# Kernel optimization log

Hardware: AMD Instinct MI355X
Metric: run time of the kernel (lower is better)

## Reference

```python
import jax, jax.numpy as jnp
import numpy as np

B, S, D, UNITS = 8, 2048, 1024, 1024

def setup_inputs() -> dict:
    key = jax.random.key(0)
    k1, k2, k3, k4 = jax.random.split(key, 4)
    scale = 1.0 / np.sqrt(D)
    return {
        "inputs": jax.random.normal(k1, (B, S, D), dtype=jnp.float32),
        "Wq": jax.random.normal(k2, (D, UNITS), dtype=jnp.float32) * scale,
        "Wk": jax.random.normal(k3, (D, UNITS), dtype=jnp.float32) * scale,
        "Wv": jax.random.normal(k4, (D, UNITS), dtype=jnp.float32) * scale,
    }

def reference(inputs, Wq, Wk, Wv):
    # QKV projections (bias-free Dense): [B,S,D] @ [D,U] -> [B,S,U]
    q = jnp.einsum("bsd,du->bsu", inputs, Wq)
    k = jnp.einsum("bsd,du->bsu", inputs, Wk)
    v = jnp.einsum("bsd,du->bsu", inputs, Wv)
    # scaled dot-product scores [B,S,S]
    scores = jnp.einsum("bqu,bku->bqk", q, k) / jnp.sqrt(jnp.float32(UNITS))
    attn = jax.nn.softmax(scores, axis=-1)
    # weighted sum of values [B,S,U]
    return jnp.einsum("bqk,bku->bqu", attn, v)
```

## Files before the change

### kernel.cpp

```cpp
#include <hip/hip_runtime.h>


#define BM 128
#define BN 128
#define BK 64

typedef _Float16 half8  __attribute__((ext_vector_type(8)));
typedef _Float16 half4v __attribute__((ext_vector_type(4)));
typedef _Float16 half2v __attribute__((ext_vector_type(2)));
typedef float    floatx4 __attribute__((ext_vector_type(4)));

__device__ __forceinline__ void stage_async(const _Float16* __restrict__ src, int ld,
                                            _Float16* __restrict__ dst, int wave, int lane) {
#pragma unroll
    for (int i = 0; i < 4; ++i) {
        int chunk = i * 4 + wave;
        int L = chunk * 64 + lane;
        int row = L >> 3, c8 = L & 7;
        int cg = c8 ^ (row & 7);
        __builtin_amdgcn_global_load_lds(
            (const __attribute__((address_space(1))) unsigned int*)(src + (size_t)row * ld + cg * 8),
            (__attribute__((address_space(3))) unsigned int*)(dst + chunk * 512),
            16, 0, 0);
    }
}

__device__ __forceinline__ void mfma_accum(const _Float16* __restrict__ As,
                                           const _Float16* __restrict__ Bs,
                                           int wm, int wn, int l15, int q4,
                                           floatx4 acc[4][4]) {
#pragma unroll
    for (int kk = 0; kk < 2; ++kk) {
        half8 a[4], b[4];
#pragma unroll
        for (int i = 0; i < 4; ++i) {
            int row = wm * 64 + i * 16 + l15;
            int cg = (kk * 4 + q4) ^ (row & 7);
            a[i] = *(const half8*)(As + row * 64 + cg * 8);
        }
#pragma unroll
        for (int j = 0; j < 4; ++j) {
            int row = wn * 64 + j * 16 + l15;
            int cg = (kk * 4 + q4) ^ (row & 7);
            b[j] = *(const half8*)(Bs + row * 64 + cg * 8);
        }
#pragma unroll
        for (int i = 0; i < 4; ++i)
#pragma unroll
            for (int j = 0; j < 4; ++j)
                acc[i][j] = __builtin_amdgcn_mfma_f32_16x16x32_f16(a[i], b[j], acc[i][j], 0, 0, 0);
    }
}

__device__ __forceinline__ float sum8h(half8 a) {
    union { half8 v; half2v h2[4]; } u; u.v = a;
    half2v s0 = u.h2[0] + u.h2[1];
    half2v s1 = u.h2[2] + u.h2[3];
    half2v s  = s0 + s1;
    return (float)s[0] + (float)s[1];
}

__global__ void cast_x(const float* __restrict__ X, _Float16* __restrict__ Xh) {
    size_t i = ((size_t)blockIdx.x * 256 + threadIdx.x) * 8;
    float4 v0 = *(const float4*)(X + i);
    float4 v1 = *(const float4*)(X + i + 4);
    half8 hh;
    hh[0] = (_Float16)v0.x; hh[1] = (_Float16)v0.y; hh[2] = (_Float16)v0.z; hh[3] = (_Float16)v0.w;
    hh[4] = (_Float16)v1.x; hh[5] = (_Float16)v1.y; hh[6] = (_Float16)v1.z; hh[7] = (_Float16)v1.w;
    *(half8*)(Xh + i) = hh;
}

__global__ void prep_weights(const float* __restrict__ Wq, const float* __restrict__ Wk,
                             const float* __restrict__ Wv, _Float16* __restrict__ WbT) {
    int g = blockIdx.z;
    const float* W = (g == 0) ? Wq : (g == 1) ? Wk : Wv;
    __shared__ float tile[32][33];
    int u0 = blockIdx.x * 32, d0 = blockIdx.y * 32;
    int tx = threadIdx.x & 31, ty = threadIdx.x >> 5;
#pragma unroll
    for (int i = 0; i < 32; i += 8)
        tile[ty + i][tx] = W[(size_t)(d0 + ty + i) * 1024 + (u0 + tx)];
    __syncthreads();
#pragma unroll
    for (int i = 0; i < 32; i += 8)
        WbT[(size_t)g * 1024 * 1024 + (size_t)(u0 + ty + i) * 1024 + (d0 + tx)] =
            (_Float16)tile[tx][ty + i];
}

__global__ void qkv_gemm(const _Float16* __restrict__ Xh, const _Float16* __restrict__ WbT,
                         _Float16* __restrict__ Qh, _Float16* __restrict__ Kh,
                         _Float16* __restrict__ Vt) {
    __shared__ __align__(16) _Float16 As[BM * BK];
    __shared__ __align__(16) _Float16 Bs[BN * BK];
    int t = threadIdx.x;
    int lane = t & 63, wave = t >> 6;
    int wm = wave >> 1, wn = wave & 1;
    int l15 = lane & 15, q4 = lane >> 4;
    int m0 = blockIdx.y * BM, n0 = blockIdx.x * BN;
    floatx4 acc[4][4] = {};
    for (int kt = 0; kt < 1024; kt += BK) {
        __syncthreads();
        stage_async(Xh + (size_t)m0 * 1024 + kt, 1024, As, wave, lane);
        stage_async(WbT + (size_t)n0 * 1024 + kt, 1024, Bs, wave, lane);
        __syncthreads();
        mfma_accum(As, Bs, wm, wn, l15, q4, acc);
    }
    int which = blockIdx.x >> 3;
    int u0 = (blockIdx.x & 7) * BN;
    int b = m0 >> 11;
    int sbase = (m0 & 2047) + wm * 64;
    if (which < 2) {
        _Float16* dst = which ? Kh : Qh;
        _Float16* db = dst + (size_t)b * 2048 * 1024;
#pragma unroll
        for (int i = 0; i < 4; ++i)
#pragma unroll
            for (int j = 0; j < 4; ++j)
#pragma unroll
                for (int r = 0; r < 4; ++r) {
                    int s = sbase + i * 16 + q4 * 4 + r;
                    int u = u0 + wn * 64 + j * 16 + l15;
                    db[(size_t)s * 1024 + u] = (_Float16)acc[i][j][r];
                }
    } else {
        _Float16* vb = Vt + (size_t)b * 1024 * 2048;
#pragma unroll
        for (int i = 0; i < 4; ++i)
#pragma unroll
            for (int j = 0; j < 4; ++j) {
                int s = sbase + i * 16 + q4 * 4;
                int u = u0 + wn * 64 + j * 16 + l15;
                half4v pk;
#pragma unroll
                for (int r = 0; r < 4; ++r) pk[r] = (_Float16)acc[i][j][r];
                *(half4v*)(vb + (size_t)u * 2048 + s) = pk;
            }
    }
}

__global__ void scores_gemm(const _Float16* __restrict__ Qh, const _Float16* __restrict__ Kh,
                            _Float16* __restrict__ P) {
    __shared__ __align__(16) _Float16 As[BM * BK];
    __shared__ __align__(16) _Float16 Bs[BN * BK];
    int t = threadIdx.x;
    int lane = t & 63, wave = t >> 6;
    int wm = wave >> 1, wn = wave & 1;
    int l15 = lane & 15, q4 = lane >> 4;
    int m0 = blockIdx.y * BM, n0 = blockIdx.x * BN;
    int batch = blockIdx.z;
    const _Float16* A = Qh + (size_t)batch * 2048 * 1024;
    const _Float16* B = Kh + (size_t)batch * 2048 * 1024;
    floatx4 acc[4][4] = {};
    for (int kt = 0; kt < 1024; kt += BK) {
        __syncthreads();
        stage_async(A + (size_t)m0 * 1024 + kt, 1024, As, wave, lane);
        stage_async(B + (size_t)n0 * 1024 + kt, 1024, Bs, wave, lane);
        __syncthreads();
        mfma_accum(As, Bs, wm, wn, l15, q4, acc);
    }
    _Float16* Pb = P + (size_t)batch * 2048 * 2048;
#pragma unroll
    for (int i = 0; i < 4; ++i)
#pragma unroll
        for (int j = 0; j < 4; ++j)
#pragma unroll
            for (int r = 0; r < 4; ++r) {
                int m = m0 + wm * 64 + i * 16 + q4 * 4 + r;
                int n = n0 + wn * 64 + j * 16 + l15;
                Pb[(size_t)m * 2048 + n] = (_Float16)__expf(acc[i][j][r] * 0.03125f);
            }
}

__global__ void pv_gemm(const _Float16* __restrict__ P, const _Float16* __restrict__ Vt,
                        float* __restrict__ out) {
    __shared__ __align__(16) _Float16 As[BM * BK];
    __shared__ __align__(16) _Float16 Bs[BN * BK];
    int t = threadIdx.x;
    int lane = t & 63, wave = t >> 6;
    int wm = wave >> 1, wn = wave & 1;
    int l15 = lane & 15, q4 = lane >> 4;
    int m0 = blockIdx.y * BM, n0 = blockIdx.x * BN;
    int batch = blockIdx.z;
    const _Float16* A = P + (size_t)batch * 2048 * 2048;
    const _Float16* B = Vt + (size_t)batch * 1024 * 2048;
    floatx4 acc[4][4] = {};
    float rsum[4] = {0.f, 0.f, 0.f, 0.f};
    for (int kt = 0; kt < 2048; kt += BK) {
        __syncthreads();
        stage_async(A + (size_t)m0 * 2048 + kt, 2048, As, wave, lane);
        stage_async(B + (size_t)n0 * 2048 + kt, 2048, Bs, wave, lane);
        __syncthreads();
#pragma unroll
        for (int kk = 0; kk < 2; ++kk) {
            half8 a[4], b[4];
#pragma unroll
            for (int i = 0; i < 4; ++i) {
                int row = wm * 64 + i * 16 + l15;
                int cg = (kk * 4 + q4) ^ (row & 7);
                a[i] = *(const half8*)(As + row * 64 + cg * 8);
                rsum[i] += sum8h(a[i]);
            }
#pragma unroll
            for (int j = 0; j < 4; ++j) {
                int row = wn * 64 + j * 16 + l15;
                int cg = (kk * 4 + q4) ^ (row & 7);
                b[j] = *(const half8*)(Bs + row * 64 + cg * 8);
            }
#pragma unroll
            for (int i = 0; i < 4; ++i)
#pragma unroll
                for (int j = 0; j < 4; ++j)
                    acc[i][j] = __builtin_amdgcn_mfma_f32_16x16x32_f16(a[i], b[j], acc[i][j], 0, 0, 0);
        }
    }
    float rsumf[4];
#pragma unroll
    for (int i = 0; i < 4; ++i) {
        float v = rsum[i] + __shfl_xor(rsum[i], 16);
        rsumf[i] = v + __shfl_xor(v, 32);
    }
    float* ob = out + (size_t)batch * 2048 * 1024;
#pragma unroll
    for (int i = 0; i < 4; ++i)
#pragma unroll
        for (int r = 0; r < 4; ++r) {
            int rloc = q4 * 4 + r;
            float inv = 1.0f / __shfl(rsumf[i], rloc);
            int m = m0 + wm * 64 + i * 16 + rloc;
#pragma unroll
            for (int j = 0; j < 4; ++j) {
                int n = n0 + wn * 64 + j * 16 + l15;
                ob[(size_t)m * 1024 + n] = acc[i][j][r] * inv;
            }
        }
}

extern "C" void kernel_launch(void* const* d_in, const int* in_sizes, int n_in,
                              void* d_out, int out_size, void* d_ws, size_t ws_size,
                              hipStream_t stream) {
    const float* X  = (const float*)d_in[0];
    const float* Wq = (const float*)d_in[1];
    const float* Wk = (const float*)d_in[2];
    const float* Wv = (const float*)d_in[3];
    float* out = (float*)d_out;

    char* ws = (char*)d_ws;
    size_t off = 0;
    _Float16* Xh  = (_Float16*)(ws + off); off += (size_t)8 * 2048 * 1024 * 2;
    _Float16* WbT = (_Float16*)(ws + off); off += (size_t)3 * 1024 * 1024 * 2;
    _Float16* Qh  = (_Float16*)(ws + off); off += (size_t)8 * 2048 * 1024 * 2;
    _Float16* Kh  = (_Float16*)(ws + off); off += (size_t)8 * 2048 * 1024 * 2;
    _Float16* Vt  = (_Float16*)(ws + off); off += (size_t)8 * 1024 * 2048 * 2;
    _Float16* P   = (_Float16*)(ws + off); off += (size_t)8 * 2048 * 2048 * 2;

    cast_x      <<<dim3(8192, 1, 1), 256, 0, stream>>>(X, Xh);
    prep_weights<<<dim3(32, 32, 3), 256, 0, stream>>>(Wq, Wk, Wv, WbT);
    qkv_gemm    <<<dim3(24, 128, 1), 256, 0, stream>>>(Xh, WbT, Qh, Kh, Vt);
    scores_gemm <<<dim3(16, 16, 8),  256, 0, stream>>>(Qh, Kh, P);
    pv_gemm     <<<dim3(8, 16, 8),   256, 0, stream>>>(P, Vt, out);
}
```

Measured before the change: 394.0 us.

## Use 256x256 tiles with 8 waves and double-buffered pipelined LDS staging

Replaces the 128x128 single-buffered GEMM loop with a shared 256x256-tile, 512-thread GEMM core. It double-buffers LDS and issues global-to-LDS loads for the next two k-steps interleaved with MFMA phases, using explicit vmcnt waits, barriers and setprio. All three GEMM stages use this core, which aims to raise arithmetic intensity and hide load latency behind compute. In exchange it uses 128KB of LDS per block and more accumulator registers, launches fewer blocks (e.g. 256 for pv), and depends on carefully ordered waits for correctness.

```diff
diff --git a/kernel.cpp b/kernel.cpp
--- a/kernel.cpp
+++ b/kernel.cpp
@@ -1,54 +1,23 @@
 #include <hip/hip_runtime.h>
 
-
-#define BM 128
-#define BN 128
-#define BK 64
 
 typedef _Float16 half8  __attribute__((ext_vector_type(8)));
 typedef _Float16 half4v __attribute__((ext_vector_type(4)));
 typedef _Float16 half2v __attribute__((ext_vector_type(2)));
 typedef float    floatx4 __attribute__((ext_vector_type(4)));
 
-__device__ __forceinline__ void stage_async(const _Float16* __restrict__ src, int ld,
-                                            _Float16* __restrict__ dst, int wave, int lane) {
-#pragma unroll
-    for (int i = 0; i < 4; ++i) {
-        int chunk = i * 4 + wave;
-        int L = chunk * 64 + lane;
-        int row = L >> 3, c8 = L & 7;
+__device__ __forceinline__ void stage_ht(const _Float16* __restrict__ src, int ld,
+                                         _Float16* __restrict__ dst, int wave, int lane) {
+#pragma unroll
+    for (int i = 0; i < 2; ++i) {
+        int q = wave * 2 + i;
+        int c = q * 64 + lane;
+        int row = c >> 3, c8 = c & 7;
         int cg = c8 ^ (row & 7);
         __builtin_amdgcn_global_load_lds(
             (const __attribute__((address_space(1))) unsigned int*)(src + (size_t)row * ld + cg * 8),
-            (__attribute__((address_space(3))) unsigned int*)(dst + chunk * 512),
+            (__attribute__((address_space(3))) unsigned int*)(dst + q * 512),
             16, 0, 0);
-    }
-}
-
-__device__ __forceinline__ void mfma_accum(const _Float16* __restrict__ As,
-                                           const _Float16* __restrict__ Bs,
-                                           int wm, int wn, int l15, int q4,
-                                           floatx4 acc[4][4]) {
-#pragma unroll
-    for (int kk = 0; kk < 2; ++kk) {
-        half8 a[4], b[4];
-#pragma unroll
-        for (int i = 0; i < 4; ++i) {
-            int row = wm * 64 + i * 16 + l15;
-            int cg = (kk * 4 + q4) ^ (row & 7);
-            a[i] = *(const half8*)(As + row * 64 + cg * 8);
-        }
-#pragma unroll
-        for (int j = 0; j < 4; ++j) {
-            int row = wn * 64 + j * 16 + l15;
-            int cg = (kk * 4 + q4) ^ (row & 7);
-            b[j] = *(const half8*)(Bs + row * 64 + cg * 8);
-        }
-#pragma unroll
-        for (int i = 0; i < 4; ++i)
-#pragma unroll
-            for (int j = 0; j < 4; ++j)
-                acc[i][j] = __builtin_amdgcn_mfma_f32_16x16x32_f16(a[i], b[j], acc[i][j], 0, 0, 0);
     }
 }
 
@@ -58,6 +27,96 @@
     half2v s1 = u.h2[2] + u.h2[3];
     half2v s  = s0 + s1;
     return (float)s[0] + (float)s[1];
+}
+
+#define SA_(T, h) stage_ht(A + (size_t)((h) * 128) * lda + (size_t)(T) * 64, lda, \
+                           ShA + (((T) & 1) * 2 + (h)) * 8192, wave, lane)
+#define SB_(T, h) stage_ht(B + (size_t)((h) * 128) * ldb + (size_t)(T) * 64, ldb, \
+                           ShB + (((T) & 1) * 2 + (h)) * 8192, wave, lane)
+
+#define LOADA(aq, i0)                                                        \
+    _Pragma("unroll")                                                        \
+    for (int ii = 0; ii < 2; ++ii) {                                         \
+        int rr = ((i0) + ii) * 16 + l15;                                     \
+        _Pragma("unroll")                                                    \
+        for (int kk = 0; kk < 2; ++kk) {                                     \
+            int cg = (kk * 4 + q4) ^ (rr & 7);                               \
+            aq[ii][kk] = *(const half8*)(As + rr * 64 + cg * 8);             \
+            if (RSUM) rsum[(i0) + ii] += sum8h(aq[ii][kk]);                  \
+        }                                                                    \
+    }
+
+#define MFMAQ(aq, i0)                                                        \
+    asm volatile("s_waitcnt lgkmcnt(0)" ::: "memory");                       \
+    __builtin_amdgcn_s_setprio(1);                                           \
+    _Pragma("unroll")                                                        \
+    for (int kk = 0; kk < 2; ++kk)                                           \
+        _Pragma("unroll")                                                    \
+        for (int ii = 0; ii < 2; ++ii)                                       \
+            _Pragma("unroll")                                                \
+            for (int j = 0; j < 4; ++j)                                      \
+                acc[(i0) + ii][j] = __builtin_amdgcn_mfma_f32_16x16x32_f16(  \
+                    aq[ii][kk], b[j][kk], acc[(i0) + ii][j], 0, 0, 0);       \
+    __builtin_amdgcn_s_setprio(0);
+
+#define BARF() do { __builtin_amdgcn_s_barrier(); asm volatile("" ::: "memory"); } while (0)
+
+template<bool RSUM>
+__device__ __forceinline__ void gemm8p(const _Float16* __restrict__ A, int lda,
+                                       const _Float16* __restrict__ B, int ldb,
+                                       int K, _Float16* __restrict__ ShA,
+                                       _Float16* __restrict__ ShB,
+                                       int wave, int lane,
+                                       floatx4 (&acc)[8][4], float (&rsum)[8]) {
+    const int wm = wave >> 2, wn = wave & 3;
+    const int l15 = lane & 15, q4 = lane >> 4;
+    const int NT = K >> 6;
+
+    SB_(0, 0); SB_(0, 1); SA_(0, 1); SA_(0, 0);
+    if (NT > 1) { SB_(1, 0); SB_(1, 1); SA_(1, 1); }
+
+    for (int t = 0; t < NT; ++t) {
+        const _Float16* As = ShA + (t & 1) * 16384 + wm * 8192;
+        const _Float16* Bs = ShB + (t & 1) * 16384 + (wn >> 1) * 8192;
+        const int rb = (wn & 1) * 64;
+        half8 b[4][2];
+        half8 a0[2][2], a1[2][2], a2[2][2], a3[2][2];
+
+        if (t + 1 < NT) SA_(t + 1, 0);
+        if (t == NT - 1) asm volatile("s_waitcnt vmcnt(0)" ::: "memory");
+        else             asm volatile("s_waitcnt vmcnt(8)" ::: "memory");
+        BARF();
+#pragma unroll
+        for (int j = 0; j < 4; ++j) {
+            int rr = rb + j * 16 + l15;
+#pragma unroll
+            for (int kk = 0; kk < 2; ++kk) {
+                int cg = (kk * 4 + q4) ^ (rr & 7);
+                b[j][kk] = *(const half8*)(Bs + rr * 64 + cg * 8);
+            }
+        }
+        LOADA(a0, 0);
+        MFMAQ(a0, 0);
+        BARF();
+
+        LOADA(a1, 2);
+        if (t + 2 < NT) SB_(t + 2, 0);
+        BARF();
+        MFMAQ(a1, 2);
+        BARF();
+
+        LOADA(a2, 4);
+        LOADA(a3, 6);
+        if (t + 2 < NT) SB_(t + 2, 1);
+        BARF();
+        MFMAQ(a2, 4);
+        BARF();
+
+        if (t + 2 < NT) SA_(t + 2, 1);
+        BARF();
+        MFMAQ(a3, 6);
+        BARF();
+    }
 }
 
 __global__ void cast_x(const float* __restrict__ X, _Float16* __restrict__ Xh) {
@@ -87,33 +146,31 @@
             (_Float16)tile[tx][ty + i];
 }
 
-__global__ void qkv_gemm(const _Float16* __restrict__ Xh, const _Float16* __restrict__ WbT,
-                         _Float16* __restrict__ Qh, _Float16* __restrict__ Kh,
-                         _Float16* __restrict__ Vt) {
-    __shared__ __align__(16) _Float16 As[BM * BK];
-    __shared__ __align__(16) _Float16 Bs[BN * BK];
+__global__ __launch_bounds__(512, 2)
+void qkv_gemm(const _Float16* __restrict__ Xh, const _Float16* __restrict__ WbT,
+              _Float16* __restrict__ Qh, _Float16* __restrict__ Kh,
+              _Float16* __restrict__ Vt) {
+    __shared__ __align__(16) _Float16 ShA[32768];
+    __shared__ __align__(16) _Float16 ShB[32768];
     int t = threadIdx.x;
     int lane = t & 63, wave = t >> 6;
-    int wm = wave >> 1, wn = wave & 1;
+    int wm = wave >> 2, wn = wave & 3;
     int l15 = lane & 15, q4 = lane >> 4;
-    int m0 = blockIdx.y * BM, n0 = blockIdx.x * BN;
-    floatx4 acc[4][4] = {};
-    for (int kt = 0; kt < 1024; kt += BK) {
-        __syncthreads();
-        stage_async(Xh + (size_t)m0 * 1024 + kt, 1024, As, wave, lane);
-        stage_async(WbT + (size_t)n0 * 1024 + kt, 1024, Bs, wave, lane);
-        __syncthreads();
-        mfma_accum(As, Bs, wm, wn, l15, q4, acc);
-    }
-    int which = blockIdx.x >> 3;
-    int u0 = (blockIdx.x & 7) * BN;
-    int b = m0 >> 11;
-    int sbase = (m0 & 2047) + wm * 64;
+    int which = blockIdx.x >> 2;
+    int u0 = (blockIdx.x & 3) * 256;
+    int m0 = blockIdx.y * 256;
+    const _Float16* A = Xh + (size_t)m0 * 1024;
+    const _Float16* B = WbT + (size_t)which * 1024 * 1024 + (size_t)u0 * 1024;
+    floatx4 acc[8][4] = {};
+    float rsum[8] = {};
+    gemm8p<false>(A, 1024, B, 1024, 1024, ShA, ShB, wave, lane, acc, rsum);
+
+    int bz = m0 >> 11;
+    int sbase = (m0 & 2047) + wm * 128;
     if (which < 2) {
-        _Float16* dst = which ? Kh : Qh;
-        _Float16* db = dst + (size_t)b * 2048 * 1024;
-#pragma unroll
-        for (int i = 0; i < 4; ++i)
+        _Float16* db = (which ? Kh : Qh) + (size_t)bz * 2048 * 1024;
+#pragma unroll
+        for (int i = 0; i < 8; ++i)
 #pragma unroll
             for (int j = 0; j < 4; ++j)
 #pragma unroll
@@ -123,9 +180,9 @@
                     db[(size_t)s * 1024 + u] = (_Float16)acc[i][j][r];
                 }
     } else {
-        _Float16* vb = Vt + (size_t)b * 1024 * 2048;
-#pragma unroll
-        for (int i = 0; i < 4; ++i)
+        _Float16* vb = Vt + (size_t)bz * 1024 * 2048;
+#pragma unroll
+        for (int i = 0; i < 8; ++i)
 #pragma unroll
             for (int j = 0; j < 4; ++j) {
                 int s = sbase + i * 16 + q4 * 4;
@@ -138,95 +195,67 @@
     }
 }
 
-__global__ void scores_gemm(const _Float16* __restrict__ Qh, const _Float16* __restrict__ Kh,
-                            _Float16* __restrict__ P) {
-    __shared__ __align__(16) _Float16 As[BM * BK];
-    __shared__ __align__(16) _Float16 Bs[BN * BK];
+__global__ __launch_bounds__(512, 2)
+void scores_gemm(const _Float16* __restrict__ Qh, const _Float16* __restrict__ Kh,
+                 _Float16* __restrict__ P) {
+    __shared__ __align__(16) _Float16 ShA[32768];
+    __shared__ __align__(16) _Float16 ShB[32768];
     int t = threadIdx.x;
     int lane = t & 63, wave = t >> 6;
-    int wm = wave >> 1, wn = wave & 1;
+    int wm = wave >> 2, wn = wave & 3;
     int l15 = lane & 15, q4 = lane >> 4;
-    int m0 = blockIdx.y * BM, n0 = blockIdx.x * BN;
+    int m0 = blockIdx.y * 256, n0 = blockIdx.x * 256;
     int batch = blockIdx.z;
-    const _Float16* A = Qh + (size_t)batch * 2048 * 1024;
-    const _Float16* B = Kh + (size_t)batch * 2048 * 1024;
-    floatx4 acc[4][4] = {};
-    for (int kt = 0; kt < 1024; kt += BK) {
-        __syncthreads();
-        stage_async(A + (size_t)m0 * 1024 + kt, 1024, As, wave, lane);
-        stage_async(B + (size_t)n0 * 1024 + kt, 1024, Bs, wave, lane);
-        __syncthreads();
-        mfma_accum(As, Bs, wm, wn, l15, q4, acc);
-    }
+    const _Float16* A = Qh + (size_t)batch * 2048 * 1024 + (size_t)m0 * 1024;
+    const _Float16* B = Kh + (size_t)batch * 2048 * 1024 + (size_t)n0 * 1024;
+    floatx4 acc[8][4] = {};
+    float rsum[8] = {};
+    gemm8p<false>(A, 1024, B, 1024, 1024, ShA, ShB, wave, lane, acc, rsum);
+
     _Float16* Pb = P + (size_t)batch * 2048 * 2048;
 #pragma unroll
-    for (int i = 0; i < 4; ++i)
+    for (int i = 0; i < 8; ++i)
 #pragma unroll
         for (int j = 0; j < 4; ++j)
 #pragma unroll
             for (int r = 0; r < 4; ++r) {
-                int m = m0 + wm * 64 + i * 16 + q4 * 4 + r;
+                int m = m0 + wm * 128 + i * 16 + q4 * 4 + r;
                 int n = n0 + wn * 64 + j * 16 + l15;
                 Pb[(size_t)m * 2048 + n] = (_Float16)__expf(acc[i][j][r] * 0.03125f);
             }
 }
 
-__global__ void pv_gemm(const _Float16* __restrict__ P, const _Float16* __restrict__ Vt,
-                        float* __restrict__ out) {
-    __shared__ __align__(16) _Float16 As[BM * BK];
-    __shared__ __align__(16) _Float16 Bs[BN * BK];
+__global__ __launch_bounds__(512, 2)
+void pv_gemm(const _Float16* __restrict__ P, const _Float16* __restrict__ Vt,
+             float* __restrict__ out) {
+    __shared__ __align__(16) _Float16 ShA[32768];
+    __shared__ __align__(16) _Float16 ShB[32768];
     int t = threadIdx.x;
     int lane = t & 63, wave = t >> 6;
-    int wm = wave >> 1, wn = wave & 1;
+    int wm = wave >> 2, wn = wave & 3;
     int l15 = lane & 15, q4 = lane >> 4;
-    int m0 = blockIdx.y * BM, n0 = blockIdx.x * BN;
+    int m0 = blockIdx.y * 256, n0 = blockIdx.x * 256;
     int batch = blockIdx.z;
-    const _Float16* A = P + (size_t)batch * 2048 * 2048;
-    const _Float16* B = Vt + (size_t)batch * 1024 * 2048;
-    floatx4 acc[4][4] = {};
-    float rsum[4] = {0.f, 0.f, 0.f, 0.f};
-    for (int kt = 0; kt < 2048; kt += BK) {
-        __syncthreads();
-        stage_async(A + (size_t)m0 * 2048 + kt, 2048, As, wave, lane);
-        stage_async(B + (size_t)n0 * 2048 + kt, 2048, Bs, wave, lane);
-        __syncthreads();
-#pragma unroll
-        for (int kk = 0; kk < 2; ++kk) {
-            half8 a[4], b[4];
-#pragma unroll
-            for (int i = 0; i < 4; ++i) {
-                int row = wm * 64 + i * 16 + l15;
-                int cg = (kk * 4 + q4) ^ (row & 7);
-                a[i] = *(const half8*)(As + row * 64 + cg * 8);
-                rsum[i] += sum8h(a[i]);
-            }
-#pragma unroll
-            for (int j = 0; j < 4; ++j) {
-                int row = wn * 64 + j * 16 + l15;
-                int cg = (kk * 4 + q4) ^ (row & 7);
-                b[j] = *(const half8*)(Bs + row * 64 + cg * 8);
-            }
-#pragma unroll
-            for (int i = 0; i < 4; ++i)
-#pragma unroll
-                for (int j = 0; j < 4; ++j)
-                    acc[i][j] = __builtin_amdgcn_mfma_f32_16x16x32_f16(a[i], b[j], acc[i][j], 0, 0, 0);
-        }
-    }
-    float rsumf[4];
-#pragma unroll
-    for (int i = 0; i < 4; ++i) {
+    const _Float16* A = P + (size_t)batch * 2048 * 2048 + (size_t)m0 * 2048;
+    const _Float16* B = Vt + (size_t)batch * 1024 * 2048 + (size_t)n0 * 2048;
+    floatx4 acc[8][4] = {};
+    float rsum[8] = {};
+    gemm8p<true>(A, 2048, B, 2048, 2048, ShA, ShB, wave, lane, acc, rsum);
+
+    float rsumf[8];
+#pragma unroll
+    for (int i = 0; i < 8; ++i) {
         float v = rsum[i] + __shfl_xor(rsum[i], 16);
         rsumf[i] = v + __shfl_xor(v, 32);
     }
     float* ob = out + (size_t)batch * 2048 * 1024;
 #pragma unroll
-    for (int i = 0; i < 4; ++i)
+    for (int i = 0; i < 8; ++i)
 #pragma unroll
         for (int r = 0; r < 4; ++r) {
             int rloc = q4 * 4 + r;
             float inv = 1.0f / __shfl(rsumf[i], rloc);
-            int m = m0 + wm * 64 + i * 16 + rloc;
+            int m = m0 + wm * 128 + i * 16 + rloc;
 #pragma unroll
             for (int j = 0; j < 4; ++j) {
                 int n = n0 + wn * 64 + j * 16 + l15;
@@ -255,7 +284,7 @@
 
     cast_x      <<<dim3(8192, 1, 1), 256, 0, stream>>>(X, Xh);
     prep_weights<<<dim3(32, 32, 3), 256, 0, stream>>>(Wq, Wk, Wv, WbT);
-    qkv_gemm    <<<dim3(24, 128, 1), 256, 0, stream>>>(Xh, WbT, Qh, Kh, Vt);
-    scores_gemm <<<dim3(16, 16, 8),  256, 0, stream>>>(Qh, Kh, P);
-    pv_gemm     <<<dim3(8, 16, 8),   256, 0, stream>>>(P, Vt, out);
-}
+    qkv_gemm    <<<dim3(12, 64, 1), 512, 0, stream>>>(Xh, WbT, Qh, Kh, Vt);
+    scores_gemm <<<dim3(8, 8, 8),   512, 0, stream>>>(Qh, Kh, P);
+    pv_gemm     <<<dim3(4, 8, 8),   512, 0, stream>>>(P, Vt, out);
+}
```

After: 452.7 us. 1.15x slower.

## Use two waves per block with 64x128 warp tiles in all GEMMs

Applied to the files above, without the earlier changes.

Halves the block size from four waves to two, giving each wave a 64x128 output tile (4x8 MFMA accumulators) instead of 64x64. Staging loops are rebalanced so each wave issues 8 async LDS loads. The intent is more MFMAs per LDS fragment load and less redundant A reuse overhead. The cost is doubled accumulator registers (128 VGPRs for acc), which may lower occupancy or cause spills, and fewer waves available to hide latency.

```diff
diff --git a/kernel.cpp b/kernel.cpp
--- a/kernel.cpp
+++ b/kernel.cpp
@@ -13,8 +13,8 @@
 __device__ __forceinline__ void stage_async(const _Float16* __restrict__ src, int ld,
                                             _Float16* __restrict__ dst, int wave, int lane) {
 #pragma unroll
-    for (int i = 0; i < 4; ++i) {
-        int chunk = i * 4 + wave;
+    for (int i = 0; i < 8; ++i) {
+        int chunk = wave * 8 + i;
         int L = chunk * 64 + lane;
         int row = L >> 3, c8 = L & 7;
         int cg = c8 ^ (row & 7);
@@ -27,11 +27,11 @@
 
 __device__ __forceinline__ void mfma_accum(const _Float16* __restrict__ As,
                                            const _Float16* __restrict__ Bs,
-                                           int wm, int wn, int l15, int q4,
-                                           floatx4 acc[4][4]) {
+                                           int wm, int l15, int q4,
+                                           floatx4 acc[4][8]) {
 #pragma unroll
     for (int kk = 0; kk < 2; ++kk) {
-        half8 a[4], b[4];
+        half8 a[4], b[8];
 #pragma unroll
         for (int i = 0; i < 4; ++i) {
             int row = wm * 64 + i * 16 + l15;
@@ -39,15 +39,15 @@
             a[i] = *(const half8*)(As + row * 64 + cg * 8);
         }
 #pragma unroll
-        for (int j = 0; j < 4; ++j) {
-            int row = wn * 64 + j * 16 + l15;
+        for (int j = 0; j < 8; ++j) {
+            int row = j * 16 + l15;
             int cg = (kk * 4 + q4) ^ (row & 7);
             b[j] = *(const half8*)(Bs + row * 64 + cg * 8);
         }
 #pragma unroll
         for (int i = 0; i < 4; ++i)
 #pragma unroll
-            for (int j = 0; j < 4; ++j)
+            for (int j = 0; j < 8; ++j)
                 acc[i][j] = __builtin_amdgcn_mfma_f32_16x16x32_f16(a[i], b[j], acc[i][j], 0, 0, 0);
     }
 }
@@ -87,23 +87,24 @@
             (_Float16)tile[tx][ty + i];
 }
 
-__global__ void qkv_gemm(const _Float16* __restrict__ Xh, const _Float16* __restrict__ WbT,
-                         _Float16* __restrict__ Qh, _Float16* __restrict__ Kh,
-                         _Float16* __restrict__ Vt) {
+__global__ __launch_bounds__(128, 2)
+void qkv_gemm(const _Float16* __restrict__ Xh, const _Float16* __restrict__ WbT,
+              _Float16* __restrict__ Qh, _Float16* __restrict__ Kh,
+              _Float16* __restrict__ Vt) {
     __shared__ __align__(16) _Float16 As[BM * BK];
     __shared__ __align__(16) _Float16 Bs[BN * BK];
     int t = threadIdx.x;
     int lane = t & 63, wave = t >> 6;
-    int wm = wave >> 1, wn = wave & 1;
+    int wm = wave;
     int l15 = lane & 15, q4 = lane >> 4;
     int m0 = blockIdx.y * BM, n0 = blockIdx.x * BN;
-    floatx4 acc[4][4] = {};
+    floatx4 acc[4][8] = {};
     for (int kt = 0; kt < 1024; kt += BK) {
         __syncthreads();
         stage_async(Xh + (size_t)m0 * 1024 + kt, 1024, As, wave, lane);
         stage_async(WbT + (size_t)n0 * 1024 + kt, 1024, Bs, wave, lane);
         __syncthreads();
-        mfma_accum(As, Bs, wm, wn, l15, q4, acc);
+        mfma_accum(As, Bs, wm, l15, q4, acc);
     }
     int which = blockIdx.x >> 3;
     int u0 = (blockIdx.x & 7) * BN;
@@ -115,11 +116,11 @@
 #pragma unroll
         for (int i = 0; i < 4; ++i)
 #pragma unroll
-            for (int j = 0; j < 4; ++j)
+            for (int j = 0; j < 8; ++j)
 #pragma unroll
                 for (int r = 0; r < 4; ++r) {
                     int s = sbase + i * 16 + q4 * 4 + r;
-                    int u = u0 + wn * 64 + j * 16 + l15;
+                    int u = u0 + j * 16 + l15;
                     db[(size_t)s * 1024 + u] = (_Float16)acc[i][j][r];
                 }
     } else {
@@ -127,9 +128,9 @@
 #pragma unroll
         for (int i = 0; i < 4; ++i)
 #pragma unroll
-            for (int j = 0; j < 4; ++j) {
+            for (int j = 0; j < 8; ++j) {
                 int s = sbase + i * 16 + q4 * 4;
-                int u = u0 + wn * 64 + j * 16 + l15;
+                int u = u0 + j * 16 + l15;
                 half4v pk;
 #pragma unroll
                 for (int r = 0; r < 4; ++r) pk[r] = (_Float16)acc[i][j][r];
@@ -138,52 +139,54 @@
     }
 }
 
-__global__ void scores_gemm(const _Float16* __restrict__ Qh, const _Float16* __restrict__ Kh,
-                            _Float16* __restrict__ P) {
+__global__ __launch_bounds__(128, 2)
+void scores_gemm(const _Float16* __restrict__ Qh, const _Float16* __restrict__ Kh,
+                 _Float16* __restrict__ P) {
     __shared__ __align__(16) _Float16 As[BM * BK];
     __shared__ __align__(16) _Float16 Bs[BN * BK];
     int t = threadIdx.x;
     int lane = t & 63, wave = t >> 6;
-    int wm = wave >> 1, wn = wave & 1;
+    int wm = wave;
     int l15 = lane & 15, q4 = lane >> 4;
     int m0 = blockIdx.y * BM, n0 = blockIdx.x * BN;
     int batch = blockIdx.z;
     const _Float16* A = Qh + (size_t)batch * 2048 * 1024;
     const _Float16* B = Kh + (size_t)batch * 2048 * 1024;
-    floatx4 acc[4][4] = {};
+    floatx4 acc[4][8] = {};
     for (int kt = 0; kt < 1024; kt += BK) {
         __syncthreads();
         stage_async(A + (size_t)m0 * 1024 + kt, 1024, As, wave, lane);
         stage_async(B + (size_t)n0 * 1024 + kt, 1024, Bs, wave, lane);
         __syncthreads();
-        mfma_accum(As, Bs, wm, wn, l15, q4, acc);
+        mfma_accum(As, Bs, wm, l15, q4, acc);
     }
     _Float16* Pb = P + (size_t)batch * 2048 * 2048;
 #pragma unroll
     for (int i = 0; i < 4; ++i)
 #pragma unroll
-        for (int j = 0; j < 4; ++j)
+        for (int j = 0; j < 8; ++j)
 #pragma unroll
             for (int r = 0; r < 4; ++r) {
                 int m = m0 + wm * 64 + i * 16 + q4 * 4 + r;
-                int n = n0 + wn * 64 + j * 16 + l15;
+                int n = n0 + j * 16 + l15;
                 Pb[(size_t)m * 2048 + n] = (_Float16)__expf(acc[i][j][r] * 0.03125f);
             }
 }
 
-__global__ void pv_gemm(const _Float16* __restrict__ P, const _Float16* __restrict__ Vt,
-                        float* __restrict__ out) {
+__global__ __launch_bounds__(128, 2)
+void pv_gemm(const _Float16* __restrict__ P, const _Float16* __restrict__ Vt,
+             float* __restrict__ out) {
     __shared__ __align__(16) _Float16 As[BM * BK];
     __shared__ __align__(16) _Float16 Bs[BN * BK];
     int t = threadIdx.x;
     int lane = t & 63, wave = t >> 6;
-    int wm = wave >> 1, wn = wave & 1;
+    int wm = wave;
     int l15 = lane & 15, q4 = lane >> 4;
     int m0 = blockIdx.y * BM, n0 = blockIdx.x * BN;
     int batch = blockIdx.z;
     const _Float16* A = P + (size_t)batch * 2048 * 2048;
     const _Float16* B = Vt + (size_t)batch * 1024 * 2048;
-    floatx4 acc[4][4] = {};
+    floatx4 acc[4][8] = {};
     float rsum[4] = {0.f, 0.f, 0.f, 0.f};
     for (int kt = 0; kt < 2048; kt += BK) {
         __syncthreads();
@@ -192,7 +195,7 @@
         __syncthreads();
 #pragma unroll
         for (int kk = 0; kk < 2; ++kk) {
-            half8 a[4], b[4];
+            half8 a[4], b[8];
 #pragma unroll
             for (int i = 0; i < 4; ++i) {
                 int row = wm * 64 + i * 16 + l15;
@@ -201,15 +204,15 @@
                 rsum[i] += sum8h(a[i]);
             }
 #pragma unroll
-            for (int j = 0; j < 4; ++j) {
-                int row = wn * 64 + j * 16 + l15;
+            for (int j = 0; j < 8; ++j) {
+                int row = j * 16 + l15;
                 int cg = (kk * 4 + q4) ^ (row & 7);
                 b[j] = *(const half8*)(Bs + row * 64 + cg * 8);
             }
 #pragma unroll
             for (int i = 0; i < 4; ++i)
 #pragma unroll
-                for (int j = 0; j < 4; ++j)
+                for (int j = 0; j < 8; ++j)
                     acc[i][j] = __builtin_amdgcn_mfma_f32_16x16x32_f16(a[i], b[j], acc[i][j], 0, 0, 0);
         }
     }
@@ -228,8 +231,8 @@
             float inv = 1.0f / __shfl(rsumf[i], rloc);
             int m = m0 + wm * 64 + i * 16 + rloc;
 #pragma unroll
-            for (int j = 0; j < 4; ++j) {
-                int n = n0 + wn * 64 + j * 16 + l15;
+            for (int j = 0; j < 8; ++j) {
+                int n = n0 + j * 16 + l15;
                 ob[(size_t)m * 1024 + n] = acc[i][j][r] * inv;
             }
         }
@@ -255,7 +258,7 @@
 
     cast_x      <<<dim3(8192, 1, 1), 256, 0, stream>>>(X, Xh);
     prep_weights<<<dim3(32, 32, 3), 256, 0, stream>>>(Wq, Wk, Wv, WbT);
-    qkv_gemm    <<<dim3(24, 128, 1), 256, 0, stream>>>(Xh, WbT, Qh, Kh, Vt);
-    scores_gemm <<<dim3(16, 16, 8),  256, 0, stream>>>(Qh, Kh, P);
-    pv_gemm     <<<dim3(8, 16, 8),   256, 0, stream>>>(P, Vt, out);
-}
+    qkv_gemm    <<<dim3(24, 128, 1), 128, 0, stream>>>(Xh, WbT, Qh, Kh, Vt);
+    scores_gemm <<<dim3(16, 16, 8), 128, 0, stream>>>(Qh, Kh, P);
+    pv_gemm     <<<dim3(8, 16, 8),  128, 0, stream>>>(P, Vt, out);
+}
```

New measurement: 422.7 us. 7.3% more time.
